# Performance work log

Hardware: AMD Instinct MI355X
Metric: run time of the kernel (lower is better)

## Reference

```python
import jax, jax.numpy as jnp
import numpy as np

N_NODES = 50000
N_EDGES = 800000
D_IN = 128
HIDDEN = 128
N_CLASSES = 40


def _sage_conv(x, edge_index, W_l, b_l, W_r, num_nodes):
    # PyG SAGEConv (aggr='mean'): out = lin_l(mean_j x_src_j) + lin_r(x_dst)
    src, dst = edge_index[0], edge_index[1]
    msg = x[src]                                              # [E, D] gather
    agg = jax.ops.segment_sum(msg, dst, num_segments=num_nodes)
    deg = jax.ops.segment_sum(jnp.ones((edge_index.shape[1],), x.dtype), dst,
                              num_segments=num_nodes)
    agg = agg / jnp.maximum(deg, 1.0)[:, None]                # scatter-mean
    return agg @ W_l + b_l + x @ W_r


def setup_inputs() -> dict:
    key = jax.random.key(0)
    k1, k2, k3, k4, k5, k6, k7 = jax.random.split(key, 7)
    s1 = 1.0 / np.sqrt(D_IN)
    s2 = 1.0 / np.sqrt(HIDDEN)
    return {
        "x": jax.random.normal(k1, (N_NODES, D_IN), dtype=jnp.float32),
        "edge_index": jax.random.randint(k2, (2, N_EDGES), 0, N_NODES, dtype=jnp.int64),
        "W1_l": jax.random.uniform(k3, (D_IN, HIDDEN), jnp.float32, -s1, s1),
        "b1": jnp.zeros((HIDDEN,), jnp.float32),
        "W1_r": jax.random.uniform(k4, (D_IN, HIDDEN), jnp.float32, -s1, s1),
        "W2_l": jax.random.uniform(k5, (HIDDEN, N_CLASSES), jnp.float32, -s2, s2),
        "b2": jnp.zeros((N_CLASSES,), jnp.float32),
        "W2_r": jax.random.uniform(k6, (HIDDEN, N_CLASSES), jnp.float32, -s2, s2),
    }


def reference(x, edge_index, W1_l, b1, W1_r, W2_l, b2, W2_r):
    # eval mode: F.dropout(training=False) is identity
    h = _sage_conv(x, edge_index, W1_l, b1, W1_r, N_NODES)
    h = jax.nn.relu(h)
    out = _sage_conv(h, edge_index, W2_l, b2, W2_r, N_NODES)
    return out
```

## Files before the change

kernel.cpp:

```cpp
#include <hip/hip_runtime.h>
#include <hip/hip_fp8.h>

#define N_NODES 50000
#define N_EDGES 800000
#define D_IN 128
#define HIDDEN 128
#define N_CLASSES 40

#define M_PAD 50048
#define CAP 64
#define EDGE_BATCH_BLOCKS 391
#define GEMM1_BLOCKS (M_PAD / 64)
#define FUSE_BLOCKS (EDGE_BATCH_BLOCKS + GEMM1_BLOCKS)

typedef __attribute__((ext_vector_type(8))) short short8;
typedef __attribute__((ext_vector_type(4))) float floatx4;

static __device__ __forceinline__ unsigned short f2bf(float f) {
    unsigned u = __float_as_uint(f);
    u = (u + 0x7fffu + ((u >> 16) & 1u)) >> 16;
    return (unsigned short)u;
}
static __device__ __forceinline__ float bf2f(unsigned short b) {
    return __uint_as_float(((unsigned)b) << 16);
}
static __device__ __forceinline__ unsigned char f2fp8(float v) {
    __hip_fp8_e4m3 t(v);
    return (unsigned char)t.__x;
}
static __device__ __forceinline__ float fp82f(unsigned char b) {
    __hip_fp8_e4m3 t;
    t.__x = (__hip_fp8_storage_t)b;
    return (float)t;
}

#define KP_W1 128
#define KP_W2 40
#define KP_CNT 196
#define KP_GRID (KP_W1 + KP_W2 + KP_CNT)

__global__ __launch_bounds__(256) void prep_kernel(
    const float* __restrict__ W1l, const float* __restrict__ W1r,
    unsigned short* __restrict__ Wt1, const float* __restrict__ W2l,
    const float* __restrict__ W2r, unsigned short* __restrict__ Wt2,
    int* __restrict__ cnt) {
    int b = blockIdx.x;
    int t = threadIdx.x;
    if (b < KP_W1) {
        int i = b * 256 + t;
        int n = i >> 7, k = i & 127;
        float v = (n < 128) ? W1l[k * 128 + n] : W1r[k * 128 + (n - 128)];
        Wt1[n * 128 + k] = f2bf(v);
    } else if (b < KP_W1 + KP_W2) {
        int i = (b - KP_W1) * 256 + t;
        int n = i >> 7, k = i & 127;
        float v = (n < 40) ? W2l[k * 40 + n] : W2r[k * 40 + (n - 40)];
        Wt2[n * 128 + k] = f2bf(v);
    } else {
        int i = (b - KP_W1 - KP_W2) * 256 + t;
        if (i < N_NODES) cnt[i] = 0;
    }
}

#define A_LD 136

__global__ __launch_bounds__(256) void fused_build_gemm1_kernel(
    const int* __restrict__ src, const int* __restrict__ dst,
    int* __restrict__ cnt, unsigned short* __restrict__ bucket,
    const float* __restrict__ x, const unsigned short* __restrict__ Wt,
    unsigned char* __restrict__ ylb, unsigned short* __restrict__ yrb) {
    __shared__ unsigned short sA[64][A_LD];

    if (blockIdx.x < EDGE_BATCH_BLOCKS) {
        int i0 = (blockIdx.x * 256 + threadIdx.x) * 8;
        if (i0 >= N_EDGES) return;
        int4 d0 = *(const int4*)(dst + i0);
        int4 d1 = *(const int4*)(dst + i0 + 4);
        int4 s0 = *(const int4*)(src + i0);
        int4 s1 = *(const int4*)(src + i0 + 4);
        int p0 = atomicAdd(&cnt[d0.x], 1);
        int p1 = atomicAdd(&cnt[d0.y], 1);
        int p2 = atomicAdd(&cnt[d0.z], 1);
        int p3 = atomicAdd(&cnt[d0.w], 1);
        int p4 = atomicAdd(&cnt[d1.x], 1);
        int p5 = atomicAdd(&cnt[d1.y], 1);
        int p6 = atomicAdd(&cnt[d1.z], 1);
        int p7 = atomicAdd(&cnt[d1.w], 1);
        if (p0 < CAP) bucket[d0.x * CAP + p0] = (unsigned short)s0.x;
        if (p1 < CAP) bucket[d0.y * CAP + p1] = (unsigned short)s0.y;
        if (p2 < CAP) bucket[d0.z * CAP + p2] = (unsigned short)s0.z;
        if (p3 < CAP) bucket[d0.w * CAP + p3] = (unsigned short)s0.w;
        if (p4 < CAP) bucket[d1.x * CAP + p4] = (unsigned short)s1.x;
        if (p5 < CAP) bucket[d1.y * CAP + p5] = (unsigned short)s1.y;
        if (p6 < CAP) bucket[d1.z * CAP + p6] = (unsigned short)s1.z;
        if (p7 < CAP) bucket[d1.w * CAP + p7] = (unsigned short)s1.w;
        return;
    }

    const int wave = threadIdx.x >> 6;
    const int lane = threadIdx.x & 63;
    const int r = lane & 15, q = lane >> 4;
    const int m0 = (blockIdx.x - EDGE_BATCH_BLOCKS) * 64;
    const int n0 = wave * 64;
    const int t = threadIdx.x;

#pragma unroll
    for (int i = 0; i < 8; i++) {
        int g = t + i * 256;
        int row = g >> 5;
        int k4 = (g & 31) << 2;
        int gr = m0 + row;
        if (gr >= N_NODES) gr = N_NODES - 1;
        float4 v = *(const float4*)(x + (size_t)gr * 128 + k4);
        uint2 p;
        p.x = (unsigned)f2bf(v.x) | ((unsigned)f2bf(v.y) << 16);
        p.y = (unsigned)f2bf(v.z) | ((unsigned)f2bf(v.w) << 16);
        *(uint2*)&sA[row][k4] = p;
    }
    __syncthreads();

    floatx4 acc[4][4];
#pragma unroll
    for (int i = 0; i < 4; i++)
#pragma unroll
        for (int j = 0; j < 4; j++) acc[i][j] = (floatx4){0.f, 0.f, 0.f, 0.f};

#pragma unroll
    for (int kc = 0; kc < 128; kc += 32) {
        short8 a[4], bb[4];
#pragma unroll
        for (int mi = 0; mi < 4; mi++)
            a[mi] = *(const short8*)&sA[mi * 16 + r][kc + q * 8];
#pragma unroll
        for (int ni = 0; ni < 4; ni++)
            bb[ni] = *(const short8*)(Wt + (size_t)(n0 + ni * 16 + r) * 128 + kc + q * 8);
#pragma unroll
        for (int mi = 0; mi < 4; mi++)
#pragma unroll
            for (int ni = 0; ni < 4; ni++)
                acc[mi][ni] = __builtin_amdgcn_mfma_f32_16x16x32_bf16(
                    a[mi], bb[ni], acc[mi][ni], 0, 0, 0);
    }

#pragma unroll
    for (int mi = 0; mi < 4; mi++) {
        int rowb = m0 + mi * 16 + q * 4;
#pragma unroll
        for (int ni = 0; ni < 4; ni++) {
            int col = n0 + ni * 16 + r;
#pragma unroll
            for (int reg = 0; reg < 4; reg++) {
                int gr = rowb + reg;
                if (gr < N_NODES) {
                    float v = acc[mi][ni][reg];
                    if (col < 128)
                        ylb[(size_t)gr * 128 + col] = f2fp8(v);
                    else
                        yrb[(size_t)gr * 128 + (col - 128)] = f2bf(v);
                }
            }
        }
    }
}

__global__ __launch_bounds__(256) void agg_gemm2_kernel(
    const unsigned short* __restrict__ yl8, const int* __restrict__ cnt,
    const unsigned short* __restrict__ bucket, const float2* __restrict__ b12,
    const unsigned int* __restrict__ yru, const unsigned short* __restrict__ Wt,
    unsigned short* __restrict__ zlb, unsigned short* __restrict__ zrb) {
    __shared__ unsigned short sH[64][A_LD];

    const int wave = threadIdx.x >> 6;
    const int l = threadIdx.x & 63;
    const int nodeBase = blockIdx.x * 64;

    for (int nd = 0; nd < 16; nd++) {
        const int lrow = wave * 16 + nd;
        int n = nodeBase + lrow;
        if (n >= N_NODES) n = N_NODES - 1;
        int deg = cnt[n];
        int re = min(deg, CAP);
        const unsigned short* bk = bucket + n * CAP;
        float ax = 0.f, ay = 0.f, bx = 0.f, by = 0.f;
        int e = 0;
        for (; e + 7 < re; e += 8) {
            unsigned short u[8];
#pragma unroll
            for (int j = 0; j < 8; j++) {
                int s = bk[e + j];
                u[j] = yl8[(size_t)s * 64 + l];
            }
#pragma unroll
            for (int j = 0; j < 8; j += 2) {
                ax += fp82f(u[j] & 0xff); ay += fp82f(u[j] >> 8);
                bx += fp82f(u[j + 1] & 0xff); by += fp82f(u[j + 1] >> 8);
            }
        }
        for (; e + 3 < re; e += 4) {
            int s0 = bk[e + 0], s1 = bk[e + 1], s2 = bk[e + 2], s3 = bk[e + 3];
            unsigned short u0 = yl8[(size_t)s0 * 64 + l];
            unsigned short u1 = yl8[(size_t)s1 * 64 + l];
            unsigned short u2 = yl8[(size_t)s2 * 64 + l];
            unsigned short u3 = yl8[(size_t)s3 * 64 + l];
            ax += fp82f(u0 & 0xff); ay += fp82f(u0 >> 8);
            bx += fp82f(u1 & 0xff); by += fp82f(u1 >> 8);
            ax += fp82f(u2 & 0xff); ay += fp82f(u2 >> 8);
            bx += fp82f(u3 & 0xff); by += fp82f(u3 >> 8);
        }
        for (; e < re; e++) {
            unsigned short u0 = yl8[(size_t)bk[e] * 64 + l];
            ax += fp82f(u0 & 0xff); ay += fp82f(u0 >> 8);
        }
        float inv = 1.0f / (float)max(deg, 1);
        unsigned ur = yru[(size_t)n * 64 + l];
        float2 b = b12[l];
        float ox = fmaxf((ax + bx) * inv + bf2f(ur & 0xffff) + b.x, 0.0f);
        float oy = fmaxf((ay + by) * inv + bf2f(ur >> 16) + b.y, 0.0f);
        *(unsigned*)&sH[lrow][2 * l] =
            (unsigned)f2bf(ox) | ((unsigned)f2bf(oy) << 16);
    }
    __syncthreads();

    const int r = l & 15, q = l >> 4;
    const int m0 = nodeBase + wave * 16;

    floatx4 acc[5];
#pragma unroll
    for (int i = 0; i < 5; i++) acc[i] = (floatx4){0.f, 0.f, 0.f, 0.f};

#pragma unroll
    for (int kc = 0; kc < 128; kc += 32) {
        short8 a = *(const short8*)&sH[wave * 16 + r][kc + q * 8];
        short8 b[5];
#pragma unroll
        for (int ni = 0; ni < 5; ni++)
            b[ni] = *(const short8*)(Wt + (size_t)(ni * 16 + r) * 128 + kc + q * 8);
#pragma unroll
        for (int ni = 0; ni < 5; ni++)
            acc[ni] = __builtin_amdgcn_mfma_f32_16x16x32_bf16(a, b[ni], acc[ni], 0, 0, 0);
    }

    int rowb = m0 + q * 4;
#pragma unroll
    for (int ni = 0; ni < 5; ni++) {
        int col = ni * 16 + r;
#pragma unroll
        for (int reg = 0; reg < 4; reg++) {
            int gr = rowb + reg;
            if (gr < N_NODES) {
                unsigned short v = f2bf(acc[ni][reg]);
                if (col < 40)
                    zlb[(size_t)gr * 40 + col] = v;
                else
                    zrb[(size_t)gr * 40 + (col - 40)] = v;
            }
        }
    }
}

__global__ __launch_bounds__(256) void agg_out2_kernel(
    const unsigned short* __restrict__ zlb, const unsigned short* __restrict__ zrb,
    const int* __restrict__ cnt, const unsigned short* __restrict__ bucket,
    const float* __restrict__ b2, float* __restrict__ out) {
    int n = blockIdx.x * 4 + (threadIdx.x >> 6);
    if (n >= N_NODES) return;
    int c = threadIdx.x & 63;
    if (c >= N_CLASSES) return;
    int deg = cnt[n];
    int re = min(deg, CAP);
    const unsigned short* bk = bucket + n * CAP;
    float a0 = 0.f, a1 = 0.f;
    int e = 0;
    for (; e + 3 < re; e += 4) {
        int s0 = bk[e + 0], s1 = bk[e + 1], s2 = bk[e + 2], s3 = bk[e + 3];
        float v0 = bf2f(zlb[(size_t)s0 * 40 + c]);
        float v1 = bf2f(zlb[(size_t)s1 * 40 + c]);
        float v2 = bf2f(zlb[(size_t)s2 * 40 + c]);
        float v3 = bf2f(zlb[(size_t)s3 * 40 + c]);
        a0 += v0 + v2;
        a1 += v1 + v3;
    }
    for (; e < re; e++) a0 += bf2f(zlb[(size_t)bk[e] * 40 + c]);
    float inv = 1.0f / (float)max(deg, 1);
    out[(size_t)n * 40 + c] =
        (a0 + a1) * inv + bf2f(zrb[(size_t)n * 40 + c]) + b2[c];
}

extern "C" void kernel_launch(void* const* d_in, const int* in_sizes, int n_in,
                              void* d_out, int out_size, void* d_ws, size_t ws_size,
                              hipStream_t stream) {
    const float* x   = (const float*)d_in[0];
    const int*   ei  = (const int*)d_in[1];
    const float* W1l = (const float*)d_in[2];
    const float* b1  = (const float*)d_in[3];
    const float* W1r = (const float*)d_in[4];
    const float* W2l = (const float*)d_in[5];
    const float* b2  = (const float*)d_in[6];
    const float* W2r = (const float*)d_in[7];
    float* out = (float*)d_out;

    const int* src = ei;
    const int* dst = ei + N_EDGES;

    char* ws = (char*)d_ws;
    int* cnt               = (int*)(ws);
    unsigned short* bucket = (unsigned short*)(ws + 262144);
    unsigned short* Wt1    = (unsigned short*)(ws + 6662144);
    unsigned short* Wt2    = (unsigned short*)(ws + 6727680);
    unsigned char*  ylb    = (unsigned char*)(ws + 19560448);
    unsigned short* yrb    = (unsigned short*)(ws + 25960448);
    unsigned short* zlb    = (unsigned short*)(ws + 38760448);
    unsigned short* zrb    = (unsigned short*)(ws + 42760448);

    prep_kernel<<<KP_GRID, 256, 0, stream>>>(W1l, W1r, Wt1, W2l, W2r, Wt2, cnt);

    fused_build_gemm1_kernel<<<FUSE_BLOCKS, 256, 0, stream>>>(
        src, dst, cnt, bucket, x, Wt1, ylb, yrb);

    agg_gemm2_kernel<<<GEMM1_BLOCKS, 256, 0, stream>>>(
        (const unsigned short*)ylb, cnt, bucket, (const float2*)b1,
        (const unsigned int*)yrb, Wt2, zlb, zrb);

    const int AGG_BLOCKS = (N_NODES + 3) / 4;
    agg_out2_kernel<<<AGG_BLOCKS, 256, 0, stream>>>(
        zlb, zrb, cnt, bucket, b2, out);
}
```

Measured before the change: 227.8 us.

## Shrink agg_gemm2 tiles to 32 rows with 8 waves splitting GEMM columns

Each agg_gemm2 block now covers 32 nodes with 512 threads. Every wave aggregates 4 nodes instead of 16, and the grid is twice as large. In the GEMM phase the 8 waves split the work by row block and by column slice (2 or 1 MFMA n-tiles each), where before each wave did all 5 n-tiles. The aim is more parallelism and better latency hiding for the gather-heavy aggregation, at the cost of more blocks and an uneven split of GEMM work across waves.

Result: faster. 203.7 us (-10.6%).

```diff
diff --git a/kernel.cpp b/kernel.cpp
--- a/kernel.cpp
+++ b/kernel.cpp
@@ -12,6 +12,10 @@
 #define EDGE_BATCH_BLOCKS 391
 #define GEMM1_BLOCKS (M_PAD / 64)
 #define FUSE_BLOCKS (EDGE_BATCH_BLOCKS + GEMM1_BLOCKS)
+
+#define AGG_ROWS 32
+#define AGG_NPW 4
+#define AGG_GRID (M_PAD / AGG_ROWS)
 
 typedef __attribute__((ext_vector_type(8))) short short8;
 typedef __attribute__((ext_vector_type(4))) float floatx4;
@@ -163,19 +167,58 @@
     }
 }
 
-__global__ __launch_bounds__(256) void agg_gemm2_kernel(
+template <int NI0, int NN>
+static __device__ __forceinline__ void gemm2_tile(
+    const unsigned short (*sH)[A_LD], const unsigned short* __restrict__ Wt,
+    unsigned short* __restrict__ zlb, unsigned short* __restrict__ zrb,
+    int m0, int lrow0, int r, int q) {
+    floatx4 acc[NN];
+#pragma unroll
+    for (int i = 0; i < NN; i++) acc[i] = (floatx4){0.f, 0.f, 0.f, 0.f};
+#pragma unroll
+    for (int kc = 0; kc < 128; kc += 32) {
+        short8 a = *(const short8*)&sH[lrow0 + r][kc + q * 8];
+        short8 b[NN];
+#pragma unroll
+        for (int ii = 0; ii < NN; ii++)
+            b[ii] = *(const short8*)(Wt + (size_t)((NI0 + ii) * 16 + r) * 128 +
+                                     kc + q * 8);
+#pragma unroll
+        for (int ii = 0; ii < NN; ii++)
+            acc[ii] =
+                __builtin_amdgcn_mfma_f32_16x16x32_bf16(a, b[ii], acc[ii], 0, 0, 0);
+    }
+    int rowb = m0 + q * 4;
+#pragma unroll
+    for (int ii = 0; ii < NN; ii++) {
+        int col = (NI0 + ii) * 16 + r;
+#pragma unroll
+        for (int reg = 0; reg < 4; reg++) {
+            int gr = rowb + reg;
+            if (gr < N_NODES) {
+                unsigned short v = f2bf(acc[ii][reg]);
+                if (col < 40)
+                    zlb[(size_t)gr * 40 + col] = v;
+                else
+                    zrb[(size_t)gr * 40 + (col - 40)] = v;
+            }
+        }
+    }
+}
+
+__global__ __launch_bounds__(512) void agg_gemm2_kernel(
     const unsigned short* __restrict__ yl8, const int* __restrict__ cnt,
     const unsigned short* __restrict__ bucket, const float2* __restrict__ b12,
     const unsigned int* __restrict__ yru, const unsigned short* __restrict__ Wt,
     unsigned short* __restrict__ zlb, unsigned short* __restrict__ zrb) {
-    __shared__ unsigned short sH[64][A_LD];
+    __shared__ unsigned short sH[AGG_ROWS][A_LD];
 
     const int wave = threadIdx.x >> 6;
     const int l = threadIdx.x & 63;
-    const int nodeBase = blockIdx.x * 64;
-
-    for (int nd = 0; nd < 16; nd++) {
-        const int lrow = wave * 16 + nd;
+    const int nodeBase = blockIdx.x * AGG_ROWS;
+
+    for (int nd = 0; nd < AGG_NPW; nd++) {
+        const int lrow = wave * AGG_NPW + nd;
         int n = nodeBase + lrow;
         if (n >= N_NODES) n = N_NODES - 1;
         int deg = cnt[n];
@@ -222,40 +265,18 @@
     __syncthreads();
 
     const int r = l & 15, q = l >> 4;
-    const int m0 = nodeBase + wave * 16;
-
-    floatx4 acc[5];
-#pragma unroll
-    for (int i = 0; i < 5; i++) acc[i] = (floatx4){0.f, 0.f, 0.f, 0.f};
-
-#pragma unroll
-    for (int kc = 0; kc < 128; kc += 32) {
-        short8 a = *(const short8*)&sH[wave * 16 + r][kc + q * 8];
-        short8 b[5];
-#pragma unroll
-        for (int ni = 0; ni < 5; ni++)
-            b[ni] = *(const short8*)(Wt + (size_t)(ni * 16 + r) * 128 + kc + q * 8);
-#pragma unroll
-        for (int ni = 0; ni < 5; ni++)
-            acc[ni] = __builtin_amdgcn_mfma_f32_16x16x32_bf16(a, b[ni], acc[ni], 0, 0, 0);
-    }
-
-    int rowb = m0 + q * 4;
-#pragma unroll
-    for (int ni = 0; ni < 5; ni++) {
-        int col = ni * 16 + r;
-#pragma unroll
-        for (int reg = 0; reg < 4; reg++) {
-            int gr = rowb + reg;
-            if (gr < N_NODES) {
-                unsigned short v = f2bf(acc[ni][reg]);
-                if (col < 40)
-                    zlb[(size_t)gr * 40 + col] = v;
-                else
-                    zrb[(size_t)gr * 40 + (col - 40)] = v;
-            }
-        }
-    }
+    const int rb = wave & 1;
+    const int part = wave >> 1;
+    const int m0 = nodeBase + rb * 16;
+    const int lrow0 = rb * 16;
+    if (part == 0)
+        gemm2_tile<0, 2>(sH, Wt, zlb, zrb, m0, lrow0, r, q);
+    else if (part == 1)
+        gemm2_tile<2, 1>(sH, Wt, zlb, zrb, m0, lrow0, r, q);
+    else if (part == 2)
+        gemm2_tile<3, 1>(sH, Wt, zlb, zrb, m0, lrow0, r, q);
+    else
+        gemm2_tile<4, 1>(sH, Wt, zlb, zrb, m0, lrow0, r, q);
 }
 
 __global__ __launch_bounds__(256) void agg_out2_kernel(
@@ -317,7 +338,7 @@
     fused_build_gemm1_kernel<<<FUSE_BLOCKS, 256, 0, stream>>>(
         src, dst, cnt, bucket, x, Wt1, ylb, yrb);
 
-    agg_gemm2_kernel<<<GEMM1_BLOCKS, 256, 0, stream>>>(
+    agg_gemm2_kernel<<<AGG_GRID, 512, 0, stream>>>(
         (const unsigned short*)ylb, cnt, bucket, (const float2*)b1,
         (const unsigned int*)yrb, Wt2, zlb, zrb);
 
```
